# Kernel optimization log

Measured on AMD Instinct MI355X. Metric: run time of the kernel, lower is better.

The kernel has to match this reference:

```python
import jax, jax.numpy as jnp
import numpy as np

T_BINS = 1000  # max_time_bins
N_HEADS = 8
BIN = 64


def _ln(x, g, b):
    m = x.mean(-1, keepdims=True)
    v = ((x - m) ** 2).mean(-1, keepdims=True)
    return (x - m) / jnp.sqrt(v + 1e-5) * g + b


def _time_attn(h, td, mask, wq, bq, wk, bk, wv, bv, wo, bo, temb):
    # h: [B,S,D], td: [B,S] float, mask: [B,S] bool
    B, S, D = h.shape
    dk = D // N_HEADS
    q = (h @ wq + bq).reshape(B, S, N_HEADS, dk)
    k = (h @ wk + bk).reshape(B, S, N_HEADS, dk)
    v = (h @ wv + bv).reshape(B, S, N_HEADS, dk)
    scores = jnp.einsum('bqhd,bkhd->bhqk', q, k) / jnp.sqrt(jnp.float32(dk))
    tb = jnp.clip(td.astype(jnp.int32), 0, T_BINS - 1)
    bias = temb[tb].transpose(0, 2, 1)[:, :, None, :]  # [B,H,1,S], key-position bias
    scores = jnp.where(mask[:, None, None, :], scores + bias, -1e9)
    attn = jax.nn.softmax(scores, axis=-1)
    ctx = jnp.einsum('bhqk,bkhd->bqhd', attn, v).reshape(B, S, D)
    return ctx @ wo + bo


def _forward(x, time_deltas,
             emb_event, emb_rel, emb_abs,
             iq_w, iq_b, ik_w, ik_b, iv_w, iv_b, io_w, io_b, i_temb, i_g, i_bt,
             eq_w, eq_b, ek_w, ek_b, ev_w, ev_b, eo_w, eo_b, e_temb, e_g, e_bt,
             w1, b1, w2, b2):
    B, S = x.shape
    NB = S // BIN  # S chosen as a multiple of bin_size -> no padding
    mask = x != 0  # padding_idx = 0
    ee = emb_event.at[0].set(0.0)  # padding_idx row is zero
    rel_bins = jnp.clip(time_deltas.astype(jnp.int32), 0, T_BINS - 1)
    abs_t = jnp.cumsum(jnp.clip(time_deltas, 0.0, None), axis=1)
    abs_bins = jnp.clip(abs_t.astype(jnp.int32), 0, T_BINS - 1)
    h = ee[x] + emb_rel[rel_bins] + emb_abs[abs_bins]  # [B,S,D]
    D = h.shape[-1]
    # intra-bin attention over [B*NB, BIN]
    hi = h.reshape(B * NB, BIN, D)
    ti = time_deltas.reshape(B * NB, BIN)
    mi = mask.reshape(B * NB, BIN)
    hi = _ln(_time_attn(hi, ti, mi, iq_w, iq_b, ik_w, ik_b, iv_w, iv_b, io_w, io_b, i_temb), i_g, i_bt)
    hi = hi.reshape(B, NB, BIN, D)
    # mean pool per bin over valid tokens
    mb = mask.reshape(B, NB, BIN)
    w = mb[..., None].astype(h.dtype)
    denom = jnp.maximum(w.sum(2), 1.0)
    bin_repr = (hi * w).sum(2) / denom  # [B,NB,D]
    bin_mask = mb.any(2)
    abs_masked = jnp.where(mb, abs_t.reshape(B, NB, BIN), 0.0)
    bin_abs = abs_masked.max(2)
    bin_rel = jnp.concatenate(
        [jnp.zeros((B, 1), h.dtype), jnp.maximum(bin_abs[:, 1:] - bin_abs[:, :-1], 0.0)], axis=1)
    h_inter = _ln(_time_attn(bin_repr, bin_rel, bin_mask,
                             eq_w, eq_b, ek_w, ek_b, ev_w, ev_b, eo_w, eo_b, e_temb), e_g, e_bt)
    last_idx = jnp.clip(bin_mask.sum(1) - 1, 0, None)
    last = h_inter[jnp.arange(B), last_idx]  # [B,D]
    return jax.nn.sigmoid(jax.nn.relu(last @ w1 + b1) @ w2 + b2)  # [B,1]


def setup_inputs() -> dict:
    key = jax.random.key(0)
    ks = jax.random.split(key, 24)
    B, S, D, V = 8, 4096, 512, 20000
    sc = 1.0 / np.sqrt(D)
    f32 = jnp.float32
    inp = {
        'x': jax.random.randint(ks[0], (B, S), 0, V),
        'time_deltas': jax.random.uniform(ks[1], (B, S), f32) * 10.0,
        'emb_event': jax.random.normal(ks[2], (V, D), f32) * 0.02,
        'emb_rel': jax.random.normal(ks[3], (T_BINS, D), f32) * 0.02,
        'emb_abs': jax.random.normal(ks[4], (T_BINS, D), f32) * 0.02,
    }
    names = ['iq', 'ik', 'iv', 'io', 'eq', 'ek', 'ev', 'eo']
    for i, n in enumerate(names):
        inp[n + '_w'] = jax.random.normal(ks[5 + i], (D, D), f32) * sc
        inp[n + '_b'] = jnp.zeros((D,), f32)
    inp['i_temb'] = jax.random.normal(ks[13], (T_BINS, N_HEADS), f32) * 0.02
    inp['e_temb'] = jax.random.normal(ks[14], (T_BINS, N_HEADS), f32) * 0.02
    inp['i_g'] = jnp.ones((D,), f32); inp['i_bt'] = jnp.zeros((D,), f32)
    inp['e_g'] = jnp.ones((D,), f32); inp['e_bt'] = jnp.zeros((D,), f32)
    inp['w1'] = jax.random.normal(ks[15], (D, D // 2), f32) * sc
    inp['b1'] = jnp.zeros((D // 2,), f32)
    inp['w2'] = jax.random.normal(ks[16], (D // 2, 1), f32) * np.sqrt(2.0 / D)
    inp['b2'] = jnp.zeros((1,), f32)
    return inp


def reference(x, time_deltas, emb_event, emb_rel, emb_abs,
              iq_w, iq_b, ik_w, ik_b, iv_w, iv_b, io_w, io_b, i_temb, i_g, i_bt,
              eq_w, eq_b, ek_w, ek_b, ev_w, ev_b, eo_w, eo_b, e_temb, e_g, e_bt,
              w1, b1, w2, b2):
    return _forward(x, time_deltas, emb_event, emb_rel, emb_abs,
                    iq_w, iq_b, ik_w, ik_b, iv_w, iv_b, io_w, io_b, i_temb, i_g, i_bt,
                    eq_w, eq_b, ek_w, ek_b, ev_w, ev_b, eo_w, eo_b, e_temb, e_g, e_bt,
                    w1, b1, w2, b2)
```

## Files before the change

kernel.cpp:

```cpp
#include <hip/hip_runtime.h>


typedef __attribute__((ext_vector_type(8))) short bf16x8;
typedef __attribute__((ext_vector_type(4))) float f32x4;

#define DEVI __device__ __forceinline__

DEVI unsigned short f2bf(float f) {
  union { float f; unsigned u; } v; v.f = f;
  unsigned r = v.u + 0x7FFFu + ((v.u >> 16) & 1u);
  return (unsigned short)(r >> 16);
}
DEVI float bf2f(unsigned short u) {
  union { unsigned u; float f; } v; v.u = ((unsigned)u) << 16; return v.f;
}

#define GLOAD_LDS16(gp, lp) \
  __builtin_amdgcn_global_load_lds((const __attribute__((address_space(1))) void*)(gp), \
                                   (__attribute__((address_space(3))) void*)(lp), 16, 0, 0)

struct TPackArgs { const float* s[8]; unsigned short* d[8];
                   const float* bs[6]; float* bd[2]; };

__global__ __launch_bounds__(256) void k_tpack8(TPackArgs args) {
  __shared__ float tile[64][65];
  if (blockIdx.x == 512) {
    int t = threadIdx.x;
    for (int i = t; i < 1536; i += 256) {
      int sel = i >> 9, r = i & 511;
      args.bd[0][i] = args.bs[sel][r];
      args.bd[1][i] = args.bs[3 + sel][r];
    }
    return;
  }
  int mat = blockIdx.x >> 6;
  int tl = blockIdx.x & 63;
  const float* W = args.s[mat];
  unsigned short* Wt = args.d[mat];
  int n0 = (tl & 7) << 6, k0 = (tl >> 3) << 6;
  int t = threadIdx.x, j = t & 63, i0 = t >> 6;
#pragma unroll
  for (int rr = 0; rr < 16; ++rr) {
    int i = rr * 4 + i0;
    tile[i][j] = W[(size_t)(k0 + i) * 512 + n0 + j];
  }
  __syncthreads();
#pragma unroll
  for (int rr = 0; rr < 16; ++rr) {
    int i = rr * 4 + i0;
    Wt[(size_t)(n0 + i) * 512 + k0 + j] = f2bf(tile[j][i]);
  }
}

__global__ __launch_bounds__(64) void k_time(const float* __restrict__ td, const int* __restrict__ x,
    float* __restrict__ abs_t, float* __restrict__ bin_rel, int* __restrict__ bin_mask,
    int* __restrict__ last_idx) {
  int b = blockIdx.x, lane = threadIdx.x;
  const float* row = td + (size_t)b * 4096 + lane * 64;
  const int*   xr  = x  + (size_t)b * 4096 + lane * 64;
  float* out = abs_t + (size_t)b * 4096 + lane * 64;
  float s = 0.f;
  for (int i = 0; i < 64; ++i) s += fmaxf(row[i], 0.f);
  float pre = s;
#pragma unroll
  for (int off = 1; off < 64; off <<= 1) {
    float n = __shfl_up(pre, off, 64);
    if (lane >= off) pre += n;
  }
  float a = pre - s;
  float am = 0.f; int anyv = 0;
  for (int i = 0; i < 64; ++i) {
    a += fmaxf(row[i], 0.f);
    out[i] = a;
    if (xr[i] != 0) { am = fmaxf(am, a); anyv = 1; }
  }
  float prev = __shfl_up(am, 1, 64);
  bin_rel[b * 64 + lane] = (lane == 0) ? 0.f : fmaxf(am - prev, 0.f);
  bin_mask[b * 64 + lane] = anyv;
  unsigned long long bal = __ballot(anyv != 0);
  if (lane == 0) last_idx[b] = max(__popcll(bal) - 1, 0);
}

__global__ __launch_bounds__(256) void k_embed(const int* __restrict__ x, const float* __restrict__ td,
    const float* __restrict__ abs_t, const float* __restrict__ ee, const float* __restrict__ er,
    const float* __restrict__ ea, unsigned short* __restrict__ h) {
  int t = threadIdx.x;
  int lane = t & 63;
  int c0 = lane * 8;
#pragma unroll
  for (int it = 0; it < 4; ++it) {
    int tok = blockIdx.x * 16 + it * 4 + (t >> 6);
    int xi = x[tok];
    int rb = (int)td[tok]; rb = min(max(rb, 0), 999);
    int ab = (int)abs_t[tok]; ab = min(max(ab, 0), 999);
    const f32x4* pr = (const f32x4*)(er + (size_t)rb * 512 + c0);
    const f32x4* pa = (const f32x4*)(ea + (size_t)ab * 512 + c0);
    f32x4 s0 = pr[0] + pa[0];
    f32x4 s1 = pr[1] + pa[1];
    if (xi != 0) {
      const f32x4* pe = (const f32x4*)(ee + (size_t)xi * 512 + c0);
      s0 += pe[0]; s1 += pe[1];
    }
    bf16x8 o;
#pragma unroll
    for (int i = 0; i < 4; ++i) { o[i] = (short)f2bf(s0[i]); o[4 + i] = (short)f2bf(s1[i]); }
    *(bf16x8*)(h + (size_t)tok * 512 + c0) = o;
  }
}

DEVI bf16x8 lds_frag32(const unsigned short* buf, int r, int g) {
  int sr = r >> 1;
  int slot = (((r & 1) << 2) | g) ^ (sr & 7);
  return *(const bf16x8*)&buf[sr * 64 + slot * 8];
}

__global__ __launch_bounds__(512, 2) void k_gemm256(const unsigned short* __restrict__ A,
    const unsigned short* __restrict__ Wt, const float* __restrict__ bias,
    unsigned short* __restrict__ Cout, int N, int tiles_n) {
  __shared__ unsigned short lds[4][2][256 * 32];
  int bid = blockIdx.x;
  { int q = (int)gridDim.x >> 3; bid = (bid & 7) * q + (bid >> 3); }
  int by = bid / tiles_n, bx = bid % tiles_n;
  int m0 = by << 8, n0 = bx << 8;
  int t = threadIdx.x;
  int lane = t & 63, w = t >> 6;
  int wm = w >> 2, wn = w & 3;
  int l15 = lane & 15, l4 = lane >> 4;

  auto stageA = [&](int kt) {
    int k0 = kt << 5;
    unsigned short* dst = &lds[kt & 3][0][0];
#pragma unroll
    for (int l = 0; l < 2; ++l) {
      int pos = l * 512 + t;
      int sr = pos >> 3, slot = pos & 7;
      int gp = slot ^ (sr & 7);
      int row = sr * 2 + (gp >> 2);
      GLOAD_LDS16(&A[(size_t)(m0 + row) * 512 + k0 + (gp & 3) * 8], dst + pos * 8);
    }
  };
  auto stageB = [&](int kt) {
    int k0 = kt << 5;
    unsigned short* dst = &lds[kt & 3][1][0];
#pragma unroll
    for (int l = 0; l < 2; ++l) {
      int pos = l * 512 + t;
      int sr = pos >> 3, slot = pos & 7;
      int gp = slot ^ (sr & 7);
      int row = sr * 2 + (gp >> 2);
      GLOAD_LDS16(&Wt[(size_t)(n0 + row) * 512 + k0 + (gp & 3) * 8], dst + pos * 8);
    }
  };

  f32x4 acc[8][4] = {};
  stageA(0); stageB(0);
  stageA(1); stageB(1);
  stageA(2); stageB(2);

  for (int kt = 0; kt < 16; ++kt) {
    if (kt < 14)       asm volatile("s_waitcnt vmcnt(8)" ::: "memory");
    else if (kt == 14) asm volatile("s_waitcnt vmcnt(4)" ::: "memory");
    else               asm volatile("s_waitcnt vmcnt(0)" ::: "memory");
    __builtin_amdgcn_s_barrier();
    const unsigned short* As = &lds[kt & 3][0][0];
    const unsigned short* Bs = &lds[kt & 3][1][0];

    bf16x8 af[4], bb[4];
#pragma unroll
    for (int i = 0; i < 4; ++i) af[i] = lds_frag32(As, wm * 128 + i * 16 + l15, l4);
#pragma unroll
    for (int j = 0; j < 4; ++j) bb[j] = lds_frag32(Bs, wn * 64 + j * 16 + l15, l4);
    if (kt < 13) stageA(kt + 3);
    __builtin_amdgcn_s_barrier();
    asm volatile("s_waitcnt lgkmcnt(0)" ::: "memory");
    __builtin_amdgcn_sched_barrier(0);
    __builtin_amdgcn_s_setprio(1);
#pragma unroll
    for (int i = 0; i < 4; ++i)
#pragma unroll
      for (int j = 0; j < 4; ++j)
        acc[i][j] = __builtin_amdgcn_mfma_f32_16x16x32_bf16(af[i], bb[j], acc[i][j], 0, 0, 0);
    __builtin_amdgcn_s_setprio(0);

    bf16x8 ah[4];
#pragma unroll
    for (int i = 0; i < 4; ++i) ah[i] = lds_frag32(As, wm * 128 + 64 + i * 16 + l15, l4);
    if (kt < 13) stageB(kt + 3);
    __builtin_amdgcn_s_barrier();
    asm volatile("s_waitcnt lgkmcnt(0)" ::: "memory");
    __builtin_amdgcn_sched_barrier(0);
    __builtin_amdgcn_s_setprio(1);
#pragma unroll
    for (int i = 0; i < 4; ++i)
#pragma unroll
      for (int j = 0; j < 4; ++j)
        acc[4 + i][j] = __builtin_amdgcn_mfma_f32_16x16x32_bf16(ah[i], bb[j], acc[4 + i][j], 0, 0, 0);
    __builtin_amdgcn_s_setprio(0);
  }
#pragma unroll
  for (int i = 0; i < 8; ++i) {
    int rowb = m0 + wm * 128 + i * 16 + (l4 << 2);
#pragma unroll
    for (int j = 0; j < 4; ++j) {
      int col = n0 + wn * 64 + j * 16 + l15;
      float bv = bias[col];
#pragma unroll
      for (int r = 0; r < 4; ++r)
        Cout[(size_t)(rowb + r) * N + col] = f2bf(acc[i][j][r] + bv);
    }
  }
}

__global__ __launch_bounds__(512, 2) void k_oproj(const unsigned short* __restrict__ ctx,
    const unsigned short* __restrict__ WoT, const float* __restrict__ bo,
    const int* __restrict__ x, const float* __restrict__ g, const float* __restrict__ bt,
    unsigned short* __restrict__ bin_repr) {
  __shared__ unsigned short ldsA[4][128 * 32];
  __shared__ unsigned short ldsB[2][512 * 32];
  int bid = blockIdx.x;
  { int q = (int)gridDim.x >> 3; bid = (bid & 7) * q + (bid >> 3); }
  int m0 = bid << 7;
  int t = threadIdx.x;
  int lane = t & 63, w = t >> 6;
  int l15 = lane & 15, l4 = lane >> 4;

  auto stageA = [&](int kt) {
    int k0 = kt << 5;
    unsigned short* dst = &ldsA[kt & 3][0];
    int pos = t;
    int sr = pos >> 3, slot = pos & 7;
    int gp = slot ^ (sr & 7);
    int row = sr * 2 + (gp >> 2);
    GLOAD_LDS16(&ctx[(size_t)(m0 + row) * 512 + k0 + (gp & 3) * 8], dst + pos * 8);
  };
  auto stageB = [&](int kt) {
    int k0 = kt << 5;
    unsigned short* dst = &ldsB[kt & 1][0];
#pragma unroll
    for (int l = 0; l < 4; ++l) {
      int pos = l * 512 + t;
      int sr = pos >> 3, slot = pos & 7;
      int gp = slot ^ (sr & 7);
      int row = sr * 2 + (gp >> 2);
      GLOAD_LDS16(&WoT[(size_t)row * 512 + k0 + (gp & 3) * 8], dst + pos * 8);
    }
  };

  f32x4 acc[8][4] = {};
  stageB(0); stageA(0); stageA(1); stageA(2); stageB(1);

  for (int kt = 0; kt < 16; ++kt) {
    if (kt == 0)      asm volatile("s_waitcnt vmcnt(6)" ::: "memory");
    else if (kt < 14) asm volatile("s_waitcnt vmcnt(1)" ::: "memory");
    else              asm volatile("s_waitcnt vmcnt(0)" ::: "memory");
    __builtin_amdgcn_s_barrier();
    const unsigned short* As = &ldsA[kt & 3][0];
    const unsigned short* Bs = &ldsB[kt & 1][0];

    bf16x8 af[4], bb[4];
#pragma unroll
    for (int i = 0; i < 4; ++i) af[i] = lds_frag32(As, i * 16 + l15, l4);
#pragma unroll
    for (int j = 0; j < 4; ++j) bb[j] = lds_frag32(Bs, w * 64 + j * 16 + l15, l4);
    if (kt >= 1 && kt <= 14) stageB(kt + 1);
    __builtin_amdgcn_s_barrier();
    asm volatile("s_waitcnt lgkmcnt(0)" ::: "memory");
    __builtin_amdgcn_sched_barrier(0);
    __builtin_amdgcn_s_setprio(1);
#pragma unroll
    for (int i = 0; i < 4; ++i)
#pragma unroll
      for (int j = 0; j < 4; ++j)
        acc[i][j] = __builtin_amdgcn_mfma_f32_16x16x32_bf16(af[i], bb[j], acc[i][j], 0, 0, 0);
    __builtin_amdgcn_s_setprio(0);

    bf16x8 ah[4];
#pragma unroll
    for (int i = 0; i < 4; ++i) ah[i] = lds_frag32(As, 64 + i * 16 + l15, l4);
    if (kt <= 12) stageA(kt + 3);
    __builtin_amdgcn_s_barrier();
    asm volatile("s_waitcnt lgkmcnt(0)" ::: "memory");
    __builtin_amdgcn_sched_barrier(0);
    __builtin_amdgcn_s_setprio(1);
#pragma unroll
    for (int i = 0; i < 4; ++i)
#pragma unroll
      for (int j = 0; j < 4; ++j)
        acc[4 + i][j] = __builtin_amdgcn_mfma_f32_16x16x32_bf16(ah[i], bb[j], acc[4 + i][j], 0, 0, 0);
    __builtin_amdgcn_s_setprio(0);
  }

  __syncthreads();
  float* red   = (float*)&ldsA[0][0];
  float* meanL = red + 128 * 9;
  float* rstdL = meanL + 128;
  int*   valL  = (int*)(rstdL + 128);
  int*   cntL  = valL + 128;

  int cols[4]; float bov[4], gv[4], bv[4];
#pragma unroll
  for (int j = 0; j < 4; ++j) {
    cols[j] = w * 64 + j * 16 + l15;
    bov[j] = bo[cols[j]]; gv[j] = g[cols[j]]; bv[j] = bt[cols[j]];
  }
  if (t < 128) {
    int v = (x[m0 + t] != 0) ? 1 : 0;
    valL[t] = v;
    unsigned long long bal = __ballot(v != 0);
    if ((t & 63) == 0) cntL[t >> 6] = __popcll(bal);
  }
#pragma unroll
  for (int i = 0; i < 8; ++i)
#pragma unroll
    for (int r = 0; r < 4; ++r) {
      float s = (acc[i][0][r] + bov[0]) + (acc[i][1][r] + bov[1]) +
                (acc[i][2][r] + bov[2]) + (acc[i][3][r] + bov[3]);
#pragma unroll
      for (int off = 1; off < 16; off <<= 1) s += __shfl_xor(s, off, 64);
      if (l15 == 0) red[(i * 16 + l4 * 4 + r) * 9 + w] = s;
    }
  __syncthreads();
  if (t < 128) {
    float m = 0.f;
#pragma unroll
    for (int ww = 0; ww < 8; ++ww) m += red[t * 9 + ww];
    meanL[t] = m * (1.f / 512.f);
  }
  __syncthreads();
#pragma unroll
  for (int i = 0; i < 8; ++i)
#pragma unroll
    for (int r = 0; r < 4; ++r) {
      float m = meanL[i * 16 + l4 * 4 + r];
      float s = 0.f;
#pragma unroll
      for (int j = 0; j < 4; ++j) { float d = acc[i][j][r] + bov[j] - m; s += d * d; }
#pragma unroll
      for (int off = 1; off < 16; off <<= 1) s += __shfl_xor(s, off, 64);
      if (l15 == 0) red[(i * 16 + l4 * 4 + r) * 9 + w] = s;
    }
  __syncthreads();
  if (t < 128) {
    float vsum = 0.f;
#pragma unroll
    for (int ww = 0; ww < 8; ++ww) vsum += red[t * 9 + ww];
    rstdL[t] = rsqrtf(vsum * (1.f / 512.f) + 1e-5f);
  }
  __syncthreads();
  float p0[4] = {0.f, 0.f, 0.f, 0.f}, p1[4] = {0.f, 0.f, 0.f, 0.f};
#pragma unroll
  for (int i = 0; i < 8; ++i)
#pragma unroll
    for (int r = 0; r < 4; ++r) {
      int row = i * 16 + l4 * 4 + r;
      if (valL[row]) {
        float m = meanL[row], rs = rstdL[row];
#pragma unroll
        for (int j = 0; j < 4; ++j) {
          float y = (acc[i][j][r] + bov[j] - m) * rs * gv[j] + bv[j];
          if (i < 4) p0[j] += y; else p1[j] += y;
        }
      }
    }
#pragma unroll
  for (int j = 0; j < 4; ++j) {
    p0[j] += __shfl_xor(p0[j], 16, 64); p0[j] += __shfl_xor(p0[j], 32, 64);
    p1[j] += __shfl_xor(p1[j], 16, 64); p1[j] += __shfl_xor(p1[j], 32, 64);
  }
  float d0 = 1.f / fmaxf((float)cntL[0], 1.f);
  float d1 = 1.f / fmaxf((float)cntL[1], 1.f);
  if (l4 == 0) {
    int binr = (m0 >> 6);
#pragma unroll
    for (int j = 0; j < 4; ++j) {
      bin_repr[(size_t)binr * 512 + cols[j]]       = f2bf(p0[j] * d0);
      bin_repr[(size_t)(binr + 1) * 512 + cols[j]] = f2bf(p1[j] * d1);
    }
  }
}

__global__ __launch_bounds__(256) void k_gemm(const unsigned short* __restrict__ A,
    const unsigned short* __restrict__ Wt, const float* __restrict__ bias,
    unsigned short* __restrict__ Cout, int N, int tiles_n) {
  __shared__ unsigned short As[128 * 72];
  __shared__ unsigned short Bs[128 * 72];
  int bx = blockIdx.x % tiles_n;
  int by = blockIdx.x / tiles_n;
  int m0 = by << 7, n0 = bx << 7;
  int t = threadIdx.x;
  int lane = t & 63, w = t >> 6;
  int wm = w >> 1, wn = w & 1;
  f32x4 acc[4][4] = {};
  for (int k0 = 0; k0 < 512; k0 += 64) {
    __syncthreads();
#pragma unroll
    for (int i = 0; i < 4; ++i) {
      int idx = t + i * 256;
      int row = idx >> 3, seg = idx & 7;
      *(bf16x8*)&As[row * 72 + seg * 8] = *(const bf16x8*)&A[(size_t)(m0 + row) * 512 + k0 + seg * 8];
      *(bf16x8*)&Bs[row * 72 + seg * 8] = *(const bf16x8*)&Wt[(size_t)(n0 + row) * 512 + k0 + seg * 8];
    }
    __syncthreads();
#pragma unroll
    for (int ks = 0; ks < 2; ++ks) {
      bf16x8 af[4], bb[4];
#pragma unroll
      for (int i = 0; i < 4; ++i) {
        af[i] = *(const bf16x8*)&As[(wm * 64 + i * 16 + (lane & 15)) * 72 + ks * 32 + (lane >> 4) * 8];
        bb[i] = *(const bf16x8*)&Bs[(wn * 64 + i * 16 + (lane & 15)) * 72 + ks * 32 + (lane >> 4) * 8];
      }
#pragma unroll
      for (int i = 0; i < 4; ++i)
#pragma unroll
        for (int j = 0; j < 4; ++j)
          acc[i][j] = __builtin_amdgcn_mfma_f32_16x16x32_bf16(af[i], bb[j], acc[i][j], 0, 0, 0);
    }
  }
#pragma unroll
  for (int i = 0; i < 4; ++i) {
    int rowb = m0 + wm * 64 + i * 16 + ((lane >> 4) << 2);
#pragma unroll
    for (int j = 0; j < 4; ++j) {
      int col = n0 + wn * 64 + j * 16 + (lane & 15);
      float bv = bias[col];
#pragma unroll
      for (int r = 0; r < 4; ++r)
        Cout[(size_t)(rowb + r) * N + col] = f2bf(acc[i][j][r] + bv);
    }
  }
}

__global__ __launch_bounds__(256) void k_attn(const unsigned short* __restrict__ qkv,
    const float* __restrict__ td, const int* __restrict__ validv,
    const float* __restrict__ temb, unsigned short* __restrict__ ctx) {
  __shared__ float bias_s[4][64];
  __shared__ int valid_s[64];
  __shared__ unsigned short P_s[4][64][72];
  __shared__ unsigned short Vt_s[4][64][72];
  int blk = blockIdx.x >> 1, hg = blockIdx.x & 1;
  int t = threadIdx.x, hl = t >> 6, lane = t & 63;
  int h = hg * 4 + hl;
  size_t base = (size_t)blk * 64;
  if (t < 64) {
    valid_s[t] = (validv[base + t] != 0) ? 1 : 0;
    int tb = (int)td[base + t];
    tb = min(max(tb, 0), 999);
#pragma unroll
    for (int hh = 0; hh < 4; ++hh) bias_s[hh][t] = temb[tb * 8 + hg * 4 + hh];
  }
  {
    const unsigned short* vp = qkv + (base + lane) * 1536 + 1024 + h * 64;
#pragma unroll
    for (int f8 = 0; f8 < 8; ++f8) {
      bf16x8 v8 = *(const bf16x8*)(vp + f8 * 8);
#pragma unroll
      for (int j = 0; j < 8; ++j) Vt_s[hl][f8 * 8 + j][lane] = (unsigned short)v8[j];
    }
  }
  __syncthreads();
  bf16x8 qa[2][4], kb[2][4];
#pragma unroll
  for (int ks = 0; ks < 2; ++ks)
#pragma unroll
    for (int i = 0; i < 4; ++i) {
      int row = i * 16 + (lane & 15);
      int kk = ks * 32 + (lane >> 4) * 8;
      qa[ks][i] = *(const bf16x8*)&qkv[(base + row) * 1536 + h * 64 + kk];
      kb[ks][i] = *(const bf16x8*)&qkv[(base + row) * 1536 + 512 + h * 64 + kk];
    }
  f32x4 acc[4][4] = {};
#pragma unroll
  for (int ks = 0; ks < 2; ++ks)
#pragma unroll
    for (int i = 0; i < 4; ++i)
#pragma unroll
      for (int j = 0; j < 4; ++j)
        acc[i][j] = __builtin_amdgcn_mfma_f32_16x16x32_bf16(qa[ks][i], kb[ks][j], acc[i][j], 0, 0, 0);
#pragma unroll
  for (int i = 0; i < 4; ++i) {
#pragma unroll
    for (int r = 0; r < 4; ++r) {
      float sv[4];
#pragma unroll
      for (int j = 0; j < 4; ++j) {
        int key = j * 16 + (lane & 15);
        float s = acc[i][j][r] * 0.125f;
        sv[j] = valid_s[key] ? (s + bias_s[hl][key]) : -1e9f;
      }
      float m = fmaxf(fmaxf(sv[0], sv[1]), fmaxf(sv[2], sv[3]));
#pragma unroll
      for (int off = 1; off < 16; off <<= 1) m = fmaxf(m, __shfl_xor(m, off, 64));
      float p[4], sum = 0.f;
#pragma unroll
      for (int j = 0; j < 4; ++j) { p[j] = __expf(sv[j] - m); sum += p[j]; }
#pragma unroll
      for (int off = 1; off < 16; off <<= 1) sum += __shfl_xor(sum, off, 64);
      float inv = 1.f / sum;
      int row = i * 16 + ((lane >> 4) << 2) + r;
#pragma unroll
      for (int j = 0; j < 4; ++j) P_s[hl][row][j * 16 + (lane & 15)] = f2bf(p[j] * inv);
    }
  }
  __syncthreads();
  f32x4 acc2[4][4] = {};
#pragma unroll
  for (int ks = 0; ks < 2; ++ks) {
    bf16x8 pa[4], vb[4];
    int kk = ks * 32 + (lane >> 4) * 8;
#pragma unroll
    for (int i = 0; i < 4; ++i) {
      pa[i] = *(const bf16x8*)&P_s[hl][i * 16 + (lane & 15)][kk];
      vb[i] = *(const bf16x8*)&Vt_s[hl][i * 16 + (lane & 15)][kk];
    }
#pragma unroll
    for (int i = 0; i < 4; ++i)
#pragma unroll
      for (int j = 0; j < 4; ++j)
        acc2[i][j] = __builtin_amdgcn_mfma_f32_16x16x32_bf16(pa[i], vb[j], acc2[i][j], 0, 0, 0);
  }
#pragma unroll
  for (int i = 0; i < 4; ++i) {
    int rowb = i * 16 + ((lane >> 4) << 2);
#pragma unroll
    for (int j = 0; j < 4; ++j) {
      int col = h * 64 + j * 16 + (lane & 15);
#pragma unroll
      for (int r = 0; r < 4; ++r)
        ctx[(base + rowb + r) * 512 + col] = f2bf(acc2[i][j][r]);
    }
  }
}

__global__ __launch_bounds__(256) void k_final(const unsigned short* __restrict__ proj2,
    const int* __restrict__ last_idx, const float* __restrict__ g, const float* __restrict__ bt,
    const float* __restrict__ w1, const float* __restrict__ b1,
    const float* __restrict__ w2, const float* __restrict__ b2, float* __restrict__ outp) {
  __shared__ float row_s[512];
  __shared__ float red_s[4];
  __shared__ float red2_s[4];
  int b = blockIdx.x, t = threadIdx.x;
  const unsigned short* rp = proj2 + (size_t)(b * 64 + last_idx[b]) * 512;
  float v0 = bf2f(rp[t]), v1 = bf2f(rp[t + 256]);
  float s = v0 + v1;
#pragma unroll
  for (int off = 1; off < 64; off <<= 1) s += __shfl_xor(s, off, 64);
  if ((t & 63) == 0) red_s[t >> 6] = s;
  __syncthreads();
  float mean = (red_s[0] + red_s[1] + red_s[2] + red_s[3]) * (1.f / 512.f);
  float d0 = v0 - mean, d1 = v1 - mean;
  float vs = d0 * d0 + d1 * d1;
#pragma unroll
  for (int off = 1; off < 64; off <<= 1) vs += __shfl_xor(vs, off, 64);
  if ((t & 63) == 0) red2_s[t >> 6] = vs;
  __syncthreads();
  float rstd = rsqrtf((red2_s[0] + red2_s[1] + red2_s[2] + red2_s[3]) * (1.f / 512.f) + 1e-5f);
  row_s[t]       = d0 * rstd * g[t]       + bt[t];
  row_s[t + 256] = d1 * rstd * g[t + 256] + bt[t + 256];
  __syncthreads();
  float acc = b1[t];
  for (int k = 0; k < 512; ++k) acc += row_s[k] * w1[(size_t)k * 256 + t];
  float hv = fmaxf(acc, 0.f) * w2[t];
#pragma unroll
  for (int off = 1; off < 64; off <<= 1) hv += __shfl_xor(hv, off, 64);
  if ((t & 63) == 0) red_s[t >> 6] = hv;
  __syncthreads();
  if (t == 0) {
    float o = red_s[0] + red_s[1] + red_s[2] + red_s[3] + b2[0];
    outp[b] = 1.f / (1.f + __expf(-o));
  }
}

extern "C" void kernel_launch(void* const* d_in, const int* in_sizes, int n_in,
                              void* d_out, int out_size, void* d_ws, size_t ws_size,
                              hipStream_t stream) {
  const int*   x    = (const int*)d_in[0];
  const float* td   = (const float*)d_in[1];
  const float* ee   = (const float*)d_in[2];
  const float* er   = (const float*)d_in[3];
  const float* ea   = (const float*)d_in[4];
  const float* iq_w = (const float*)d_in[5];  const float* iq_b = (const float*)d_in[6];
  const float* ik_w = (const float*)d_in[7];  const float* ik_b = (const float*)d_in[8];
  const float* iv_w = (const float*)d_in[9];  const float* iv_b = (const float*)d_in[10];
  const float* io_w = (const float*)d_in[11]; const float* io_b = (const float*)d_in[12];
  const float* eq_w = (const float*)d_in[13]; const float* eq_b = (const float*)d_in[14];
  const float* ek_w = (const float*)d_in[15]; const float* ek_b = (const float*)d_in[16];
  const float* ev_w = (const float*)d_in[17]; const float* ev_b = (const float*)d_in[18];
  const float* eo_w = (const float*)d_in[19]; const float* eo_b = (const float*)d_in[20];
  const float* i_temb = (const float*)d_in[21];
  const float* e_temb = (const float*)d_in[22];
  const float* i_g  = (const float*)d_in[23]; const float* i_bt = (const float*)d_in[24];
  const float* e_g  = (const float*)d_in[25]; const float* e_bt = (const float*)d_in[26];
  const float* w1   = (const float*)d_in[27]; const float* b1   = (const float*)d_in[28];
  const float* w2   = (const float*)d_in[29]; const float* b2   = (const float*)d_in[30];

  char* ws = (char*)d_ws;
  size_t off = 0;
  auto alloc = [&](size_t nb) { size_t r = off; off += (nb + 255) & ~(size_t)255; return r; };
  float* abs_t    = (float*)(ws + alloc((size_t)32768 * 4));
  float* bin_rel  = (float*)(ws + alloc(512 * 4));
  int*   bin_mask = (int*)(ws + alloc(512 * 4));
  int*   last_idx = (int*)(ws + alloc(64));
  unsigned short* wqkv_i = (unsigned short*)(ws + alloc((size_t)1536 * 512 * 2));
  unsigned short* wo_i   = (unsigned short*)(ws + alloc((size_t)512 * 512 * 2));
  unsigned short* wqkv_e = (unsigned short*)(ws + alloc((size_t)1536 * 512 * 2));
  unsigned short* wo_e   = (unsigned short*)(ws + alloc((size_t)512 * 512 * 2));
  float* bqkv_i = (float*)(ws + alloc(1536 * 4));
  float* bqkv_e = (float*)(ws + alloc(1536 * 4));
  unsigned short* hbuf = (unsigned short*)(ws + alloc((size_t)32768 * 512 * 2));
  unsigned short* qkvbuf = (unsigned short*)(ws + alloc((size_t)32768 * 1536 * 2));
  unsigned short* bin_repr = (unsigned short*)(ws + alloc((size_t)512 * 512 * 2));
  char* small = ws + alloc((size_t)512 * 1536 * 2);
  unsigned short* qkv2 = (unsigned short*)small;
  unsigned short* proj2 = (unsigned short*)small;
  unsigned short* ctx2 = (unsigned short*)(ws + alloc((size_t)512 * 512 * 2));

  TPackArgs tp;
  tp.s[0] = iq_w; tp.d[0] = wqkv_i;
  tp.s[1] = ik_w; tp.d[1] = wqkv_i + (size_t)512 * 512;
  tp.s[2] = iv_w; tp.d[2] = wqkv_i + (size_t)1024 * 512;
  tp.s[3] = io_w; tp.d[3] = wo_i;
  tp.s[4] = eq_w; tp.d[4] = wqkv_e;
  tp.s[5] = ek_w; tp.d[5] = wqkv_e + (size_t)512 * 512;
  tp.s[6] = ev_w; tp.d[6] = wqkv_e + (size_t)1024 * 512;
  tp.s[7] = eo_w; tp.d[7] = wo_e;
  tp.bs[0] = iq_b; tp.bs[1] = ik_b; tp.bs[2] = iv_b;
  tp.bs[3] = eq_b; tp.bs[4] = ek_b; tp.bs[5] = ev_b;
  tp.bd[0] = bqkv_i; tp.bd[1] = bqkv_e;
  k_tpack8<<<513, 256, 0, stream>>>(tp);

  k_time<<<8, 64, 0, stream>>>(td, x, abs_t, bin_rel, bin_mask, last_idx);

  k_embed<<<2048, 256, 0, stream>>>(x, td, abs_t, ee, er, ea, hbuf);

  k_gemm256<<<128 * 6, 512, 0, stream>>>(hbuf, wqkv_i, bqkv_i, qkvbuf, 1536, 6);
  k_attn<<<1024, 256, 0, stream>>>(qkvbuf, td, x, i_temb, hbuf);
  k_oproj<<<256, 512, 0, stream>>>(hbuf, wo_i, io_b, x, i_g, i_bt, bin_repr);

  k_gemm<<<4 * 12, 256, 0, stream>>>(bin_repr, wqkv_e, bqkv_e, qkv2, 1536, 12);
  k_attn<<<16, 256, 0, stream>>>(qkv2, bin_rel, bin_mask, e_temb, ctx2);
  k_gemm<<<4 * 4, 256, 0, stream>>>(ctx2, wo_e, eo_b, proj2, 512, 4);

  k_final<<<8, 256, 0, stream>>>(proj2, last_idx, e_g, e_bt, w1, b1, w2, b2, (float*)d_out);
}
```

Baseline: 231.1 us.

## Simplify QKV and O-proj GEMMs to single-buffered 64-wide K tiles

Replaces the deeply pipelined 256x256 QKV GEMM, which used a 4-stage global_load_lds buffer and hand-placed waitcnts, with a simpler 128x128-tile kernel. That kernel stages 64-wide K chunks and syncs twice per chunk. The O-projection GEMM gets the same simpler single-buffer scheme. k_time now stages td and x through LDS with vector loads instead of strided scalar access. Attention defers softmax normalization to the output store. Together these trade the old load/compute overlap for more blocks and simpler code, and risk exposing memory latency in the GEMMs.

```diff
diff --git a/kernel.cpp b/kernel.cpp
--- a/kernel.cpp
+++ b/kernel.cpp
@@ -3,6 +3,7 @@
 
 typedef __attribute__((ext_vector_type(8))) short bf16x8;
 typedef __attribute__((ext_vector_type(4))) float f32x4;
+typedef __attribute__((ext_vector_type(4))) int i32x4;
 
 #define DEVI __device__ __forceinline__
 
@@ -55,12 +56,21 @@
 __global__ __launch_bounds__(64) void k_time(const float* __restrict__ td, const int* __restrict__ x,
     float* __restrict__ abs_t, float* __restrict__ bin_rel, int* __restrict__ bin_mask,
     int* __restrict__ last_idx) {
+  __shared__ float tds[4096];
+  __shared__ int xs[4096];
   int b = blockIdx.x, lane = threadIdx.x;
-  const float* row = td + (size_t)b * 4096 + lane * 64;
-  const int*   xr  = x  + (size_t)b * 4096 + lane * 64;
-  float* out = abs_t + (size_t)b * 4096 + lane * 64;
+  const f32x4* tp = (const f32x4*)(td + (size_t)b * 4096);
+  const i32x4* xp = (const i32x4*)(x + (size_t)b * 4096);
+  for (int j = lane; j < 1024; j += 64) {
+    f32x4 v = tp[j];
+#pragma unroll
+    for (int c = 0; c < 4; ++c) v[c] = fmaxf(v[c], 0.f);
+    *(f32x4*)&tds[j * 4] = v;
+    *(i32x4*)&xs[j * 4] = xp[j];
+  }
+  __syncthreads();
   float s = 0.f;
-  for (int i = 0; i < 64; ++i) s += fmaxf(row[i], 0.f);
+  for (int i = 0; i < 64; ++i) s += tds[lane * 64 + i];
   float pre = s;
 #pragma unroll
   for (int off = 1; off < 64; off <<= 1) {
@@ -70,10 +80,14 @@
   float a = pre - s;
   float am = 0.f; int anyv = 0;
   for (int i = 0; i < 64; ++i) {
-    a += fmaxf(row[i], 0.f);
-    out[i] = a;
-    if (xr[i] != 0) { am = fmaxf(am, a); anyv = 1; }
-  }
+    a += tds[lane * 64 + i];
+    tds[lane * 64 + i] = a;
+    if (xs[lane * 64 + i] != 0) { am = fmaxf(am, a); anyv = 1; }
+  }
+  __syncthreads();
+  float* out = abs_t + (size_t)b * 4096;
+  for (int j = lane; j < 1024; j += 64)
+    *(f32x4*)&out[j * 4] = *(const f32x4*)&tds[j * 4];
   float prev = __shfl_up(am, 1, 64);
   bin_rel[b * 64 + lane] = (lane == 0) ? 0.f : fmaxf(am - prev, 0.f);
   bin_mask[b * 64 + lane] = anyv;
@@ -108,101 +122,60 @@
   }
 }
 
-DEVI bf16x8 lds_frag32(const unsigned short* buf, int r, int g) {
-  int sr = r >> 1;
-  int slot = (((r & 1) << 2) | g) ^ (sr & 7);
-  return *(const bf16x8*)&buf[sr * 64 + slot * 8];
-}
-
-__global__ __launch_bounds__(512, 2) void k_gemm256(const unsigned short* __restrict__ A,
+DEVI bf16x8 lds_frag64(const unsigned short* buf, int row, int c) {
+  return *(const bf16x8*)&buf[row * 64 + ((c ^ (row & 7)) << 3)];
+}
+
+__global__ __launch_bounds__(256) void k_g128(const unsigned short* __restrict__ A,
     const unsigned short* __restrict__ Wt, const float* __restrict__ bias,
     unsigned short* __restrict__ Cout, int N, int tiles_n) {
-  __shared__ unsigned short lds[4][2][256 * 32];
+  __shared__ unsigned short As[128 * 64];
+  __shared__ unsigned short Bs[128 * 64];
   int bid = blockIdx.x;
   { int q = (int)gridDim.x >> 3; bid = (bid & 7) * q + (bid >> 3); }
   int by = bid / tiles_n, bx = bid % tiles_n;
-  int m0 = by << 8, n0 = bx << 8;
+  int m0 = by << 7, n0 = bx << 7;
   int t = threadIdx.x;
   int lane = t & 63, w = t >> 6;
-  int wm = w >> 2, wn = w & 3;
+  int wm = w >> 1, wn = w & 1;
   int l15 = lane & 15, l4 = lane >> 4;
-
-  auto stageA = [&](int kt) {
-    int k0 = kt << 5;
-    unsigned short* dst = &lds[kt & 3][0][0];
-#pragma unroll
-    for (int l = 0; l < 2; ++l) {
-      int pos = l * 512 + t;
-      int sr = pos >> 3, slot = pos & 7;
-      int gp = slot ^ (sr & 7);
-      int row = sr * 2 + (gp >> 2);
-      GLOAD_LDS16(&A[(size_t)(m0 + row) * 512 + k0 + (gp & 3) * 8], dst + pos * 8);
-    }
-  };
-  auto stageB = [&](int kt) {
-    int k0 = kt << 5;
-    unsigned short* dst = &lds[kt & 3][1][0];
-#pragma unroll
-    for (int l = 0; l < 2; ++l) {
-      int pos = l * 512 + t;
-      int sr = pos >> 3, slot = pos & 7;
-      int gp = slot ^ (sr & 7);
-      int row = sr * 2 + (gp >> 2);
-      GLOAD_LDS16(&Wt[(size_t)(n0 + row) * 512 + k0 + (gp & 3) * 8], dst + pos * 8);
-    }
-  };
-
-  f32x4 acc[8][4] = {};
-  stageA(0); stageB(0);
-  stageA(1); stageB(1);
-  stageA(2); stageB(2);
-
-  for (int kt = 0; kt < 16; ++kt) {
-    if (kt < 14)       asm volatile("s_waitcnt vmcnt(8)" ::: "memory");
-    else if (kt == 14) asm volatile("s_waitcnt vmcnt(4)" ::: "memory");
-    else               asm volatile("s_waitcnt vmcnt(0)" ::: "memory");
-    __builtin_amdgcn_s_barrier();
-    const unsigned short* As = &lds[kt & 3][0][0];
-    const unsigned short* Bs = &lds[kt & 3][1][0];
-
-    bf16x8 af[4], bb[4];
-#pragma unroll
-    for (int i = 0; i < 4; ++i) af[i] = lds_frag32(As, wm * 128 + i * 16 + l15, l4);
-#pragma unroll
-    for (int j = 0; j < 4; ++j) bb[j] = lds_frag32(Bs, wn * 64 + j * 16 + l15, l4);
-    if (kt < 13) stageA(kt + 3);
-    __builtin_amdgcn_s_barrier();
-    asm volatile("s_waitcnt lgkmcnt(0)" ::: "memory");
-    __builtin_amdgcn_sched_barrier(0);
-    __builtin_amdgcn_s_setprio(1);
-#pragma unroll
-    for (int i = 0; i < 4; ++i)
-#pragma unroll
-      for (int j = 0; j < 4; ++j)
-        acc[i][j] = __builtin_amdgcn_mfma_f32_16x16x32_bf16(af[i], bb[j], acc[i][j], 0, 0, 0);
-    __builtin_amdgcn_s_setprio(0);
-
-    bf16x8 ah[4];
-#pragma unroll
-    for (int i = 0; i < 4; ++i) ah[i] = lds_frag32(As, wm * 128 + 64 + i * 16 + l15, l4);
-    if (kt < 13) stageB(kt + 3);
-    __builtin_amdgcn_s_barrier();
-    asm volatile("s_waitcnt lgkmcnt(0)" ::: "memory");
-    __builtin_amdgcn_sched_barrier(0);
-    __builtin_amdgcn_s_setprio(1);
-#pragma unroll
-    for (int i = 0; i < 4; ++i)
-#pragma unroll
-      for (int j = 0; j < 4; ++j)
-        acc[4 + i][j] = __builtin_amdgcn_mfma_f32_16x16x32_bf16(ah[i], bb[j], acc[4 + i][j], 0, 0, 0);
-    __builtin_amdgcn_s_setprio(0);
-  }
-#pragma unroll
-  for (int i = 0; i < 8; ++i) {
-    int rowb = m0 + wm * 128 + i * 16 + (l4 << 2);
+  f32x4 acc[4][4] = {};
+  for (int k0 = 0; k0 < 512; k0 += 64) {
+    __syncthreads();
+#pragma unroll
+    for (int l = 0; l < 4; ++l) {
+      int pos = l * 256 + t;
+      int row = pos >> 3, g = (pos & 7) ^ (row & 7);
+      GLOAD_LDS16(&A[(size_t)(m0 + row) * 512 + k0 + g * 8], &As[pos * 8]);
+    }
+#pragma unroll
+    for (int l = 0; l < 4; ++l) {
+      int pos = l * 256 + t;
+      int row = pos >> 3, g = (pos & 7) ^ (row & 7);
+      GLOAD_LDS16(&Wt[(size_t)(n0 + row) * 512 + k0 + g * 8], &Bs[pos * 8]);
+    }
+    __syncthreads();
+#pragma unroll
+    for (int ks = 0; ks < 2; ++ks) {
+      bf16x8 af[4], bb[4];
+#pragma unroll
+      for (int i = 0; i < 4; ++i) {
+        af[i] = lds_frag64(As, wm * 64 + i * 16 + l15, ks * 4 + l4);
+        bb[i] = lds_frag64(Bs, wn * 64 + i * 16 + l15, ks * 4 + l4);
+      }
+#pragma unroll
+      for (int i = 0; i < 4; ++i)
+#pragma unroll
+        for (int j = 0; j < 4; ++j)
+          acc[i][j] = __builtin_amdgcn_mfma_f32_16x16x32_bf16(af[i], bb[j], acc[i][j], 0, 0, 0);
+    }
+  }
+#pragma unroll
+  for (int i = 0; i < 4; ++i) {
+    int rowb = m0 + wm * 64 + i * 16 + ((lane >> 4) << 2);
 #pragma unroll
     for (int j = 0; j < 4; ++j) {
-      int col = n0 + wn * 64 + j * 16 + l15;
+      int col = n0 + wn * 64 + j * 16 + (lane & 15);
       float bv = bias[col];
 #pragma unroll
       for (int r = 0; r < 4; ++r)
@@ -215,8 +188,8 @@
     const unsigned short* __restrict__ WoT, const float* __restrict__ bo,
     const int* __restrict__ x, const float* __restrict__ g, const float* __restrict__ bt,
     unsigned short* __restrict__ bin_repr) {
-  __shared__ unsigned short ldsA[4][128 * 32];
-  __shared__ unsigned short ldsB[2][512 * 32];
+  __shared__ unsigned short As[128 * 64];
+  __shared__ unsigned short Bs[512 * 64];
   int bid = blockIdx.x;
   { int q = (int)gridDim.x >> 3; bid = (bid & 7) * q + (bid >> 3); }
   int m0 = bid << 7;
@@ -224,74 +197,39 @@
   int lane = t & 63, w = t >> 6;
   int l15 = lane & 15, l4 = lane >> 4;
 
-  auto stageA = [&](int kt) {
-    int k0 = kt << 5;
-    unsigned short* dst = &ldsA[kt & 3][0];
-    int pos = t;
-    int sr = pos >> 3, slot = pos & 7;
-    int gp = slot ^ (sr & 7);
-    int row = sr * 2 + (gp >> 2);
-    GLOAD_LDS16(&ctx[(size_t)(m0 + row) * 512 + k0 + (gp & 3) * 8], dst + pos * 8);
-  };
-  auto stageB = [&](int kt) {
-    int k0 = kt << 5;
-    unsigned short* dst = &ldsB[kt & 1][0];
-#pragma unroll
-    for (int l = 0; l < 4; ++l) {
+  f32x4 acc[8][4] = {};
+  for (int k0 = 0; k0 < 512; k0 += 64) {
+    __syncthreads();
+#pragma unroll
+    for (int l = 0; l < 2; ++l) {
       int pos = l * 512 + t;
-      int sr = pos >> 3, slot = pos & 7;
-      int gp = slot ^ (sr & 7);
-      int row = sr * 2 + (gp >> 2);
-      GLOAD_LDS16(&WoT[(size_t)row * 512 + k0 + (gp & 3) * 8], dst + pos * 8);
-    }
-  };
-
-  f32x4 acc[8][4] = {};
-  stageB(0); stageA(0); stageA(1); stageA(2); stageB(1);
-
-  for (int kt = 0; kt < 16; ++kt) {
-    if (kt == 0)      asm volatile("s_waitcnt vmcnt(6)" ::: "memory");
-    else if (kt < 14) asm volatile("s_waitcnt vmcnt(1)" ::: "memory");
-    else              asm volatile("s_waitcnt vmcnt(0)" ::: "memory");
-    __builtin_amdgcn_s_barrier();
-    const unsigned short* As = &ldsA[kt & 3][0];
-    const unsigned short* Bs = &ldsB[kt & 1][0];
-
-    bf16x8 af[4], bb[4];
-#pragma unroll
-    for (int i = 0; i < 4; ++i) af[i] = lds_frag32(As, i * 16 + l15, l4);
-#pragma unroll
-    for (int j = 0; j < 4; ++j) bb[j] = lds_frag32(Bs, w * 64 + j * 16 + l15, l4);
-    if (kt >= 1 && kt <= 14) stageB(kt + 1);
-    __builtin_amdgcn_s_barrier();
-    asm volatile("s_waitcnt lgkmcnt(0)" ::: "memory");
-    __builtin_amdgcn_sched_barrier(0);
-    __builtin_amdgcn_s_setprio(1);
-#pragma unroll
-    for (int i = 0; i < 4; ++i)
-#pragma unroll
-      for (int j = 0; j < 4; ++j)
-        acc[i][j] = __builtin_amdgcn_mfma_f32_16x16x32_bf16(af[i], bb[j], acc[i][j], 0, 0, 0);
-    __builtin_amdgcn_s_setprio(0);
-
-    bf16x8 ah[4];
-#pragma unroll
-    for (int i = 0; i < 4; ++i) ah[i] = lds_frag32(As, 64 + i * 16 + l15, l4);
-    if (kt <= 12) stageA(kt + 3);
-    __builtin_amdgcn_s_barrier();
-    asm volatile("s_waitcnt lgkmcnt(0)" ::: "memory");
-    __builtin_amdgcn_sched_barrier(0);
-    __builtin_amdgcn_s_setprio(1);
-#pragma unroll
-    for (int i = 0; i < 4; ++i)
-#pragma unroll
-      for (int j = 0; j < 4; ++j)
-        acc[4 + i][j] = __builtin_amdgcn_mfma_f32_16x16x32_bf16(ah[i], bb[j], acc[4 + i][j], 0, 0, 0);
-    __builtin_amdgcn_s_setprio(0);
-  }
-
-  __syncthreads();
-  float* red   = (float*)&ldsA[0][0];
+      int row = pos >> 3, gg = (pos & 7) ^ (row & 7);
+      GLOAD_LDS16(&ctx[(size_t)(m0 + row) * 512 + k0 + gg * 8], &As[pos * 8]);
+    }
+#pragma unroll
+    for (int l = 0; l < 8; ++l) {
+      int pos = l * 512 + t;
+      int row = pos >> 3, gg = (pos & 7) ^ (row & 7);
+      GLOAD_LDS16(&WoT[(size_t)row * 512 + k0 + gg * 8], &Bs[pos * 8]);
+    }
+    __syncthreads();
+#pragma unroll
+    for (int ks = 0; ks < 2; ++ks) {
+      bf16x8 af[8], bb[4];
+#pragma unroll
+      for (int i = 0; i < 8; ++i) af[i] = lds_frag64(As, i * 16 + l15, ks * 4 + l4);
+#pragma unroll
+      for (int j = 0; j < 4; ++j) bb[j] = lds_frag64(Bs, w * 64 + j * 16 + l15, ks * 4 + l4);
+#pragma unroll
+      for (int i = 0; i < 8; ++i)
+#pragma unroll
+        for (int j = 0; j < 4; ++j)
+          acc[i][j] = __builtin_amdgcn_mfma_f32_16x16x32_bf16(af[i], bb[j], acc[i][j], 0, 0, 0);
+    }
+  }
+
+  __syncthreads();
+  float* red   = (float*)&As[0];
   float* meanL = red + 128 * 9;
   float* rstdL = meanL + 128;
   int*   valL  = (int*)(rstdL + 128);
@@ -476,6 +414,7 @@
 #pragma unroll
       for (int j = 0; j < 4; ++j)
         acc[i][j] = __builtin_amdgcn_mfma_f32_16x16x32_bf16(qa[ks][i], kb[ks][j], acc[i][j], 0, 0, 0);
+  float invs[4][4];
 #pragma unroll
   for (int i = 0; i < 4; ++i) {
 #pragma unroll
@@ -495,10 +434,10 @@
       for (int j = 0; j < 4; ++j) { p[j] = __expf(sv[j] - m); sum += p[j]; }
 #pragma unroll
       for (int off = 1; off < 16; off <<= 1) sum += __shfl_xor(sum, off, 64);
-      float inv = 1.f / sum;
+      invs[i][r] = 1.f / sum;
       int row = i * 16 + ((lane >> 4) << 2) + r;
 #pragma unroll
-      for (int j = 0; j < 4; ++j) P_s[hl][row][j * 16 + (lane & 15)] = f2bf(p[j] * inv);
+      for (int j = 0; j < 4; ++j) P_s[hl][row][j * 16 + (lane & 15)] = f2bf(p[j]);
     }
   }
   __syncthreads();
@@ -526,7 +465,7 @@
       int col = h * 64 + j * 16 + (lane & 15);
 #pragma unroll
       for (int r = 0; r < 4; ++r)
-        ctx[(base + rowb + r) * 512 + col] = f2bf(acc2[i][j][r]);
+        ctx[(base + rowb + r) * 512 + col] = f2bf(acc2[i][j][r] * invs[i][r]);
     }
   }
 }
@@ -632,7 +571,7 @@
 
   k_embed<<<2048, 256, 0, stream>>>(x, td, abs_t, ee, er, ea, hbuf);
 
-  k_gemm256<<<128 * 6, 512, 0, stream>>>(hbuf, wqkv_i, bqkv_i, qkvbuf, 1536, 6);
+  k_g128<<<256 * 12, 256, 0, stream>>>(hbuf, wqkv_i, bqkv_i, qkvbuf, 1536, 12);
   k_attn<<<1024, 256, 0, stream>>>(qkvbuf, td, x, i_temb, hbuf);
   k_oproj<<<256, 512, 0, stream>>>(hbuf, wo_i, io_b, x, i_g, i_bt, bin_repr);
 
```

After: 238.5 us. +3.2%, slower.

## Stage time scan in LDS, shrink GEMM pipeline, defer softmax normalization

Applied to the files above, without the earlier changes.

The time-scan kernel now loads time deltas and tokens into LDS with vectorized global reads, runs the scan in LDS and writes abs_t back with vector stores, instead of doing strided per-lane scalar global accesses. The GEMM pipeline drops from a 4-stage LDS ring with 3 tiles in flight to double buffering with one tile prefetched, halving LDS use but waiting on all loads every iteration. The attention kernel stores unnormalized probabilities, scales the PV result by the reciprocal row sum afterwards, and stages the context tile through LDS (reusing Vt_s) so global writes become coalesced 16-byte stores. Reusing Vt_s as scratch may race if other waves in the block still read it, since no barrier is visible before the reuse.

```diff
diff --git a/kernel.cpp b/kernel.cpp
--- a/kernel.cpp
+++ b/kernel.cpp
@@ -3,6 +3,7 @@
 
 typedef __attribute__((ext_vector_type(8))) short bf16x8;
 typedef __attribute__((ext_vector_type(4))) float f32x4;
+typedef __attribute__((ext_vector_type(4))) int i32x4;
 
 #define DEVI __device__ __forceinline__
 
@@ -55,12 +56,21 @@
 __global__ __launch_bounds__(64) void k_time(const float* __restrict__ td, const int* __restrict__ x,
     float* __restrict__ abs_t, float* __restrict__ bin_rel, int* __restrict__ bin_mask,
     int* __restrict__ last_idx) {
+  __shared__ float tds[4096];
+  __shared__ int xs[4096];
   int b = blockIdx.x, lane = threadIdx.x;
-  const float* row = td + (size_t)b * 4096 + lane * 64;
-  const int*   xr  = x  + (size_t)b * 4096 + lane * 64;
-  float* out = abs_t + (size_t)b * 4096 + lane * 64;
+  const f32x4* tp = (const f32x4*)(td + (size_t)b * 4096);
+  const i32x4* xp = (const i32x4*)(x + (size_t)b * 4096);
+  for (int j = lane; j < 1024; j += 64) {
+    f32x4 v = tp[j];
+#pragma unroll
+    for (int c = 0; c < 4; ++c) v[c] = fmaxf(v[c], 0.f);
+    *(f32x4*)&tds[j * 4] = v;
+    *(i32x4*)&xs[j * 4] = xp[j];
+  }
+  __syncthreads();
   float s = 0.f;
-  for (int i = 0; i < 64; ++i) s += fmaxf(row[i], 0.f);
+  for (int i = 0; i < 64; ++i) s += tds[lane * 64 + i];
   float pre = s;
 #pragma unroll
   for (int off = 1; off < 64; off <<= 1) {
@@ -70,10 +80,14 @@
   float a = pre - s;
   float am = 0.f; int anyv = 0;
   for (int i = 0; i < 64; ++i) {
-    a += fmaxf(row[i], 0.f);
-    out[i] = a;
-    if (xr[i] != 0) { am = fmaxf(am, a); anyv = 1; }
-  }
+    a += tds[lane * 64 + i];
+    tds[lane * 64 + i] = a;
+    if (xs[lane * 64 + i] != 0) { am = fmaxf(am, a); anyv = 1; }
+  }
+  __syncthreads();
+  float* out = abs_t + (size_t)b * 4096;
+  for (int j = lane; j < 1024; j += 64)
+    *(f32x4*)&out[j * 4] = *(const f32x4*)&tds[j * 4];
   float prev = __shfl_up(am, 1, 64);
   bin_rel[b * 64 + lane] = (lane == 0) ? 0.f : fmaxf(am - prev, 0.f);
   bin_mask[b * 64 + lane] = anyv;
@@ -117,7 +131,7 @@
 __global__ __launch_bounds__(512, 2) void k_gemm256(const unsigned short* __restrict__ A,
     const unsigned short* __restrict__ Wt, const float* __restrict__ bias,
     unsigned short* __restrict__ Cout, int N, int tiles_n) {
-  __shared__ unsigned short lds[4][2][256 * 32];
+  __shared__ unsigned short lds[2][2][256 * 32];
   int bid = blockIdx.x;
   { int q = (int)gridDim.x >> 3; bid = (bid & 7) * q + (bid >> 3); }
   int by = bid / tiles_n, bx = bid % tiles_n;
@@ -129,7 +143,7 @@
 
   auto stageA = [&](int kt) {
     int k0 = kt << 5;
-    unsigned short* dst = &lds[kt & 3][0][0];
+    unsigned short* dst = &lds[kt & 1][0][0];
 #pragma unroll
     for (int l = 0; l < 2; ++l) {
       int pos = l * 512 + t;
@@ -141,7 +155,7 @@
   };
   auto stageB = [&](int kt) {
     int k0 = kt << 5;
-    unsigned short* dst = &lds[kt & 3][1][0];
+    unsigned short* dst = &lds[kt & 1][1][0];
 #pragma unroll
     for (int l = 0; l < 2; ++l) {
       int pos = l * 512 + t;
@@ -154,23 +168,19 @@
 
   f32x4 acc[8][4] = {};
   stageA(0); stageB(0);
-  stageA(1); stageB(1);
-  stageA(2); stageB(2);
 
   for (int kt = 0; kt < 16; ++kt) {
-    if (kt < 14)       asm volatile("s_waitcnt vmcnt(8)" ::: "memory");
-    else if (kt == 14) asm volatile("s_waitcnt vmcnt(4)" ::: "memory");
-    else               asm volatile("s_waitcnt vmcnt(0)" ::: "memory");
+    asm volatile("s_waitcnt vmcnt(0)" ::: "memory");
     __builtin_amdgcn_s_barrier();
-    const unsigned short* As = &lds[kt & 3][0][0];
-    const unsigned short* Bs = &lds[kt & 3][1][0];
+    const unsigned short* As = &lds[kt & 1][0][0];
+    const unsigned short* Bs = &lds[kt & 1][1][0];
 
     bf16x8 af[4], bb[4];
 #pragma unroll
     for (int i = 0; i < 4; ++i) af[i] = lds_frag32(As, wm * 128 + i * 16 + l15, l4);
 #pragma unroll
     for (int j = 0; j < 4; ++j) bb[j] = lds_frag32(Bs, wn * 64 + j * 16 + l15, l4);
-    if (kt < 13) stageA(kt + 3);
+    if (kt < 15) stageA(kt + 1);
     __builtin_amdgcn_s_barrier();
     asm volatile("s_waitcnt lgkmcnt(0)" ::: "memory");
     __builtin_amdgcn_sched_barrier(0);
@@ -185,7 +195,7 @@
     bf16x8 ah[4];
 #pragma unroll
     for (int i = 0; i < 4; ++i) ah[i] = lds_frag32(As, wm * 128 + 64 + i * 16 + l15, l4);
-    if (kt < 13) stageB(kt + 3);
+    if (kt < 15) stageB(kt + 1);
     __builtin_amdgcn_s_barrier();
     asm volatile("s_waitcnt lgkmcnt(0)" ::: "memory");
     __builtin_amdgcn_sched_barrier(0);
@@ -476,6 +486,7 @@
 #pragma unroll
       for (int j = 0; j < 4; ++j)
         acc[i][j] = __builtin_amdgcn_mfma_f32_16x16x32_bf16(qa[ks][i], kb[ks][j], acc[i][j], 0, 0, 0);
+  float invs[4][4];
 #pragma unroll
   for (int i = 0; i < 4; ++i) {
 #pragma unroll
@@ -495,10 +506,10 @@
       for (int j = 0; j < 4; ++j) { p[j] = __expf(sv[j] - m); sum += p[j]; }
 #pragma unroll
       for (int off = 1; off < 16; off <<= 1) sum += __shfl_xor(sum, off, 64);
-      float inv = 1.f / sum;
+      invs[i][r] = 1.f / sum;
       int row = i * 16 + ((lane >> 4) << 2) + r;
 #pragma unroll
-      for (int j = 0; j < 4; ++j) P_s[hl][row][j * 16 + (lane & 15)] = f2bf(p[j] * inv);
+      for (int j = 0; j < 4; ++j) P_s[hl][row][j * 16 + (lane & 15)] = f2bf(p[j]);
     }
   }
   __syncthreads();
@@ -518,16 +529,20 @@
       for (int j = 0; j < 4; ++j)
         acc2[i][j] = __builtin_amdgcn_mfma_f32_16x16x32_bf16(pa[i], vb[j], acc2[i][j], 0, 0, 0);
   }
-#pragma unroll
-  for (int i = 0; i < 4; ++i) {
-    int rowb = i * 16 + ((lane >> 4) << 2);
-#pragma unroll
-    for (int j = 0; j < 4; ++j) {
-      int col = h * 64 + j * 16 + (lane & 15);
+  unsigned short* scr = &Vt_s[hl][0][0];
+#pragma unroll
+  for (int i = 0; i < 4; ++i)
+#pragma unroll
+    for (int j = 0; j < 4; ++j)
 #pragma unroll
       for (int r = 0; r < 4; ++r)
-        ctx[(base + rowb + r) * 512 + col] = f2bf(acc2[i][j][r]);
-    }
+        scr[(i * 16 + ((lane >> 4) << 2) + r) * 72 + j * 16 + (lane & 15)] =
+            f2bf(acc2[i][j][r] * invs[i][r]);
+#pragma unroll
+  for (int p = 0; p < 8; ++p) {
+    int rl = p * 8 + (lane >> 3);
+    bf16x8 vv = *(const bf16x8*)&scr[rl * 72 + (lane & 7) * 8];
+    *(bf16x8*)&ctx[(base + rl) * 512 + h * 64 + (lane & 7) * 8] = vv;
   }
 }
 
```

Result: no change. 228.6 us (-1.1%).
